# Kernel tuning notes

Measured on AMD Instinct MI355X. Metric: run time of the kernel, lower is better.

The kernel has to match this reference:

```python
import jax, jax.numpy as jnp
import numpy as np

B = 16384
D_IN = 1024
D_OUT = 512
H1 = 4 * D_IN      # floor(layersDimentions[0]*inputDimention) = 4096
H3 = 4 * D_OUT     # floor(layersDimentions[1]*outputDimention) = 2048
H4 = 4 * D_OUT     # floor(layersDimentions[2]*outputDimention) = 2048
M = 256            # codebook size


def _linear_params(key, fan_in, fan_out):
    kw, kb = jax.random.split(key)
    bound = 1.0 / np.sqrt(fan_in)
    w = jax.random.uniform(kw, (fan_out, fan_in), jnp.float32, -bound, bound)
    b = jax.random.uniform(kb, (fan_out,), jnp.float32, -bound, bound)
    return w, b


def setup_inputs() -> dict:
    key = jax.random.key(0)
    ks = jax.random.split(key, 7)
    x = jax.random.normal(ks[0], (B, D_IN), jnp.float32)
    codebook = jnp.sort(jax.random.normal(ks[1], (M,), jnp.float32))
    w1, b1 = _linear_params(ks[2], D_IN, H1)
    w2, b2 = _linear_params(ks[3], H1, D_OUT)
    w3, b3 = _linear_params(ks[4], D_OUT, H3)
    w4, b4 = _linear_params(ks[5], H3, H4)
    w5, b5 = _linear_params(ks[6], H4, D_OUT)
    return {"x": x, "codebook": codebook,
            "w1": w1, "b1": b1, "w2": w2, "b2": b2,
            "w3": w3, "b3": b3, "w4": w4, "b4": b4,
            "w5": w5, "b5": b5}


def _quantize(x, codebook):
    # nearest codeword per scalar element: argmin_m |x - c_m|
    # x: [B, D], codebook: [M]
    d = jnp.abs(x[..., None] - codebook)          # [B, D, M]
    idx = jnp.argmin(d, axis=-1)                  # [B, D]
    return codebook[idx]


def reference(x, codebook, w1, b1, w2, b2, w3, b3, w4, b4, w5, b5):
    h = x @ w1.T + b1                # [B, H1]
    h = h @ w2.T + b2                # [B, D_OUT]
    h = _quantize(h, codebook)       # [B, D_OUT]
    h = h @ w3.T + b3                # [B, H3]
    h = h @ w4.T + b4                # [B, H4]
    return h @ w5.T + b5             # [B, D_OUT]
```

## Files before the change

kernel.cpp:

```cpp
#include <hip/hip_runtime.h>


typedef __bf16 v8bf __attribute__((ext_vector_type(8)));
typedef float  v4f  __attribute__((ext_vector_type(4)));

#define Bdim   16384
#define DIN    1024
#define DOUT   512
#define H1dim  4096
#define H3dim  2048
#define H4dim  2048

#define GLOBAL_AS __attribute__((address_space(1)))
#define LDS_AS    __attribute__((address_space(3)))

__device__ __forceinline__ void load16_to_lds(const __bf16* g, __bf16* l) {
  __builtin_amdgcn_global_load_lds((const GLOBAL_AS unsigned int*)g,
                                   (LDS_AS unsigned int*)l, 16, 0, 0);
}

__device__ __forceinline__ unsigned pack2bf(float a, float b) {
  return (unsigned)__builtin_bit_cast(unsigned short, (__bf16)a) |
         ((unsigned)__builtin_bit_cast(unsigned short, (__bf16)b) << 16);
}

__device__ __forceinline__ void transpose_body(const float* __restrict__ in,
                                               __bf16* __restrict__ out,
                                               int R, int C, int bx, int by,
                                               float (*tile)[33]) {
  const int c0 = bx * 32, r0 = by * 32;
  const int t = threadIdx.x, tr = t >> 5, tc = t & 31;
#pragma unroll
  for (int i = 0; i < 4; ++i)
    tile[tr + i * 8][tc] = in[(size_t)(r0 + tr + i * 8) * C + (c0 + tc)];
  __syncthreads();
#pragma unroll
  for (int i = 0; i < 4; ++i)
    out[(size_t)(c0 + tr + i * 8) * R + (r0 + tc)] = (__bf16)tile[tc][tr + i * 8];
}

__global__ void prep_kernel(const float* __restrict__ w1, __bf16* __restrict__ w1T,
                            const float* __restrict__ w4, __bf16* __restrict__ w4T,
                            const float* __restrict__ w3, __bf16* __restrict__ w3T,
                            const float* __restrict__ x, __bf16* __restrict__ xb) {
  __shared__ float tile[32][33];
  int b = blockIdx.x;
  if (b < 4096) {
    transpose_body(w1, w1T, H1dim, DIN, b & 31, b >> 5, tile);
  } else if (b < 8192) {
    b -= 4096;
    transpose_body(w4, w4T, H4dim, H3dim, b & 63, b >> 6, tile);
  } else if (b < 9216) {
    b -= 8192;
    transpose_body(w3, w3T, H3dim, DOUT, b & 15, b >> 4, tile);
  } else {
    const size_t i = (size_t)(b - 9216) * 2048 + (size_t)threadIdx.x * 8;
    float4 a = *(const float4*)&x[i];
    float4 c = *(const float4*)&x[i + 4];
    int4 o;
    o.x = pack2bf(a.x, a.y); o.y = pack2bf(a.z, a.w);
    o.z = pack2bf(c.x, c.y); o.w = pack2bf(c.z, c.w);
    *(int4*)&xb[i] = o;
  }
}

__device__ __forceinline__ void bias_body(int bb, const float* __restrict__ b1,
                                          const float* __restrict__ w2,
                                          const float* __restrict__ b2,
                                          const float* __restrict__ b3,
                                          const __bf16* __restrict__ WtT,
                                          const float* __restrict__ b4,
                                          const float* __restrict__ w5,
                                          const float* __restrict__ b5,
                                          float* __restrict__ ba, float* __restrict__ bc) {
  const int wave = threadIdx.x >> 6, lane = threadIdx.x & 63;
  if (bb < 128) {
    const int j = bb * 4 + wave;
    float s = 0.f;
    for (int k = lane; k < H1dim; k += 64) s += b1[k] * w2[(size_t)j * H1dim + k];
#pragma unroll
    for (int off = 32; off; off >>= 1) s += __shfl_xor(s, off, 64);
    if (lane == 0) ba[j] = s + b2[j];
  } else {
    const int j = (bb - 128) * 4 + wave;
    float s = 0.f;
    for (int k = lane; k < H4dim; k += 64)
      s += b3[k] * (float)WtT[(size_t)j * H4dim + k] + b4[k] * w5[(size_t)j * H4dim + k];
#pragma unroll
    for (int off = 32; off; off >>= 1) s += __shfl_xor(s, off, 64);
    if (lane == 0) bc[j] = s + b5[j];
  }
}

template <bool ABF16>
__device__ __forceinline__ void splitk_body(__bf16* As, __bf16* Bs,
                                            int bx, int by, int bz,
                                            const void* __restrict__ Ain,
                                            const __bf16* __restrict__ Bt,
                                            float* __restrict__ Cpart,
                                            int M, int N, int K, int Kchunk) {
  const int t = threadIdx.x;
  const int m0 = bx * 64, n0 = by * 64;
  const int kbeg = bz * Kchunk;
  const int lane = t & 63, wave = t >> 6;
  const int quad = lane >> 4, l15 = lane & 15;
  const int wm = (wave & 1) * 32, wn = (wave >> 1) * 32;

  v4f acc[2][2];
#pragma unroll
  for (int i = 0; i < 2; ++i)
#pragma unroll
    for (int j = 0; j < 2; ++j) acc[i][j] = (v4f){0.f, 0.f, 0.f, 0.f};

  const int r = t >> 2, c = (t & 3) * 8;
  for (int k0 = kbeg; k0 < kbeg + Kchunk; k0 += 32) {
    if constexpr (ABF16) {
      const __bf16* A = (const __bf16*)Ain;
      *(int4*)&As[r * 40 + c] = *(const int4*)&A[(size_t)(m0 + r) * K + (k0 + c)];
    } else {
      const float* A = (const float*)Ain;
#pragma unroll
      for (int p = 0; p < 2; ++p) {
        const int idx = p * 256 + t;
        const int row = idx >> 3, col = (idx & 7) * 4;
        float4 v = *(const float4*)&A[(size_t)(m0 + row) * K + (k0 + col)];
        uint2 o;
        o.x = pack2bf(v.x, v.y);
        o.y = pack2bf(v.z, v.w);
        *(uint2*)&As[row * 40 + col] = o;
      }
    }
    *(int4*)&Bs[r * 40 + c] = *(const int4*)&Bt[(size_t)(n0 + r) * K + (k0 + c)];
    __syncthreads();
    v8bf af[2], bfr[2];
#pragma unroll
    for (int i = 0; i < 2; ++i) {
      af[i]  = *(const v8bf*)&As[(wm + i * 16 + l15) * 40 + quad * 8];
      bfr[i] = *(const v8bf*)&Bs[(wn + i * 16 + l15) * 40 + quad * 8];
    }
#pragma unroll
    for (int i = 0; i < 2; ++i)
#pragma unroll
      for (int j = 0; j < 2; ++j)
        acc[i][j] = __builtin_amdgcn_mfma_f32_16x16x32_bf16(af[i], bfr[j], acc[i][j], 0, 0, 0);
    __syncthreads();
  }

  float* dst = Cpart + (size_t)bz * M * N;
#pragma unroll
  for (int i = 0; i < 2; ++i)
#pragma unroll
    for (int j = 0; j < 2; ++j)
#pragma unroll
      for (int r2 = 0; r2 < 4; ++r2) {
        const int gm = m0 + wm + i * 16 + quad * 4 + r2;
        const int gn = n0 + wn + j * 16 + l15;
        dst[(size_t)gm * N + gn] = acc[i][j][r2];
      }
}

__global__ __launch_bounds__(256, 4)
void fold12_kernel(const float* __restrict__ w2, const __bf16* __restrict__ w1T,
                   float* __restrict__ part1,
                   const float* __restrict__ w5, const __bf16* __restrict__ w4T,
                   float* __restrict__ part2) {
  __shared__ __align__(16) __bf16 As[64 * 40];
  __shared__ __align__(16) __bf16 Bs[64 * 40];
  int b = blockIdx.x;
  if (b < 1024) {
    splitk_body<false>(As, Bs, b & 7, (b >> 3) & 15, b >> 7,
                       w2, w1T, part1, DOUT, DIN, H1dim, H1dim / 8);
  } else {
    b -= 1024;
    splitk_body<false>(As, Bs, b & 7, (b >> 3) & 31, b >> 8,
                       w5, w4T, part2, DOUT, H3dim, H4dim, H4dim / 4);
  }
}

__global__ __launch_bounds__(256, 4)
void fold3_bias_kernel(const __bf16* __restrict__ WtT, const __bf16* __restrict__ w3T,
                       float* __restrict__ part,
                       const float* __restrict__ b1, const float* __restrict__ w2,
                       const float* __restrict__ b2, const float* __restrict__ b3,
                       const float* __restrict__ b4, const float* __restrict__ w5,
                       const float* __restrict__ b5,
                       float* __restrict__ ba, float* __restrict__ bc) {
  __shared__ __align__(16) __bf16 As[64 * 40];
  __shared__ __align__(16) __bf16 Bs[64 * 40];
  int b = blockIdx.x;
  if (b < 512) {
    splitk_body<true>(As, Bs, b & 7, (b >> 3) & 7, b >> 6,
                      WtT, w3T, part, DOUT, DOUT, H3dim, H3dim / 8);
  } else {
    bias_body(b - 512, b1, w2, b2, b3, WtT, b4, w5, b5, ba, bc);
  }
}

__device__ __forceinline__ void reduce_body(const float* __restrict__ part,
                                            __bf16* __restrict__ out, int MN4, int S, int i) {
  if (i >= MN4) return;
  const float4* p = reinterpret_cast<const float4*>(part);
  float4 s = p[i];
  for (int k = 1; k < S; ++k) {
    float4 v = p[(size_t)k * MN4 + i];
    s.x += v.x; s.y += v.y; s.z += v.z; s.w += v.w;
  }
  uint2 o;
  o.x = pack2bf(s.x, s.y);
  o.y = pack2bf(s.z, s.w);
  reinterpret_cast<uint2*>(out)[i] = o;
}

__global__ void reduce12_kernel(const float* __restrict__ part1, __bf16* __restrict__ WaT,
                                const float* __restrict__ part2, __bf16* __restrict__ WtT) {
  const int b = blockIdx.x, t = threadIdx.x;
  if (b < 512) reduce_body(part1, WaT, DOUT * DIN / 4, 8, b * 256 + t);
  else         reduce_body(part2, WtT, DOUT * H3dim / 4, 4, (b - 512) * 256 + t);
}

__global__ void reduce_cast_kernel(const float* __restrict__ part,
                                   __bf16* __restrict__ out, int MN4, int S) {
  int i = blockIdx.x * blockDim.x + threadIdx.x;
  reduce_body(part, out, MN4, S, i);
}

enum { MODE_Q = 1, MODE_OUT = 2 };

template <int MODE>
__global__ __launch_bounds__(256, 4)
void gemm_main_kernel(const __bf16* __restrict__ A, const __bf16* __restrict__ Bt,
                      void* __restrict__ Cout, const float* __restrict__ bias,
                      const float* __restrict__ codebook, int M, int N, int K) {
  __shared__ __align__(16) __bf16 As[128 * 64];
  __shared__ __align__(16) __bf16 Bs[64 * 64];
  __shared__ float cbs[256];

  const int t = threadIdx.x;
  const int m0 = blockIdx.x * 128;
  const int n0 = blockIdx.y * 64;
  if constexpr (MODE == MODE_Q) cbs[t] = codebook[t];

  const int lane = t & 63, wave = t >> 6;
  const int quad = lane >> 4, l15 = lane & 15;
  const int wm = (wave & 1) * 64, wn = (wave >> 1) * 32;

  const int lrow = lane >> 3;
  const int gcol = (((lane & 7) ^ lrow) * 8);

  const __bf16* gA = A  + (size_t)(m0 + 32 * wave + lrow) * K + gcol;
  const __bf16* gB = Bt + (size_t)(n0 + 16 * wave + lrow) * K + gcol;
  __bf16* lA = &As[32 * wave * 64];
  __bf16* lB = &Bs[16 * wave * 64];

  v4f acc[4][2];
#pragma unroll
  for (int i = 0; i < 4; ++i)
#pragma unroll
    for (int j = 0; j < 2; ++j) acc[i][j] = (v4f){0.f, 0.f, 0.f, 0.f};

  const int swz = l15 & 7;

  for (int k0 = 0; k0 < K; k0 += 64) {
#pragma unroll
    for (int p = 0; p < 4; ++p)
      load16_to_lds(gA + (size_t)(8 * p) * K + k0, lA + p * 512);
#pragma unroll
    for (int p = 0; p < 2; ++p)
      load16_to_lds(gB + (size_t)(8 * p) * K + k0, lB + p * 512);
    __syncthreads();

#pragma unroll
    for (int kk = 0; kk < 2; ++kk) {
      const int cch = ((kk * 4 + quad) ^ swz) * 8;
      v8bf af[4], bv[2];
#pragma unroll
      for (int i = 0; i < 4; ++i)
        af[i] = *(const v8bf*)&As[(wm + i * 16 + l15) * 64 + cch];
#pragma unroll
      for (int j = 0; j < 2; ++j)
        bv[j] = *(const v8bf*)&Bs[(wn + j * 16 + l15) * 64 + cch];
#pragma unroll
      for (int i = 0; i < 4; ++i)
#pragma unroll
        for (int j = 0; j < 2; ++j)
          acc[i][j] = __builtin_amdgcn_mfma_f32_16x16x32_bf16(af[i], bv[j], acc[i][j], 0, 0, 0);
    }
    __syncthreads();
  }

#pragma unroll
  for (int j = 0; j < 2; ++j) {
    const int gn = n0 + wn + j * 16 + l15;
    const float bj = bias[gn];
#pragma unroll
    for (int i = 0; i < 4; ++i) {
#pragma unroll
      for (int r = 0; r < 4; ++r) {
        const int gm = m0 + wm + i * 16 + quad * 4 + r;
        float v = acc[i][j][r] + bj;
        if constexpr (MODE == MODE_Q) {
          int idx = 0;
#pragma unroll
          for (int s = 128; s > 0; s >>= 1) {
            const int u = idx + s;
            if (cbs[u] <= v) idx = u;
          }
          float best = cbs[idx];
          if (idx < 255) {
            const float c1 = cbs[idx + 1];
            if (!(v - best <= c1 - v)) best = c1;
          }
          ((__bf16*)Cout)[(size_t)gm * N + gn] = (__bf16)best;
        } else {
          ((float*)Cout)[(size_t)gm * N + gn] = v;
        }
      }
    }
  }
}

extern "C" void kernel_launch(void* const* d_in, const int* in_sizes, int n_in,
                              void* d_out, int out_size, void* d_ws, size_t ws_size,
                              hipStream_t stream) {
  const float* x  = (const float*)d_in[0];
  const float* cb = (const float*)d_in[1];
  const float* w1 = (const float*)d_in[2];
  const float* b1 = (const float*)d_in[3];
  const float* w2 = (const float*)d_in[4];
  const float* b2 = (const float*)d_in[5];
  const float* w3 = (const float*)d_in[6];
  const float* b3 = (const float*)d_in[7];
  const float* w4 = (const float*)d_in[8];
  const float* b4 = (const float*)d_in[9];
  const float* w5 = (const float*)d_in[10];
  const float* b5 = (const float*)d_in[11];
  float* out = (float*)d_out;

  char* ws = (char*)d_ws;
  size_t off = 0;
  auto alloc = [&](size_t bytes) -> void* {
    void* p = ws + off;
    off = (off + bytes + 255) & ~(size_t)255;
    return p;
  };
  __bf16* w1T  = (__bf16*)alloc((size_t)DIN * H1dim * 2);
  __bf16* w4T  = (__bf16*)alloc((size_t)H3dim * H4dim * 2);
  __bf16* w3T  = (__bf16*)alloc((size_t)DOUT * H3dim * 2);
  __bf16* WaT  = (__bf16*)alloc((size_t)DOUT * DIN * 2);
  __bf16* WtT  = (__bf16*)alloc((size_t)DOUT * H3dim * 2);
  __bf16* WcT  = (__bf16*)alloc((size_t)DOUT * DOUT * 2);
  __bf16* q    = (__bf16*)alloc((size_t)Bdim * DOUT * 2);
  float*  ba   = (float*)alloc(DOUT * 4);
  float*  bc   = (float*)alloc(DOUT * 4);
  float*  part1 = (float*)alloc((size_t)8 * DOUT * DIN * 4);
  __bf16* xb   = (__bf16*)alloc((size_t)Bdim * DIN * 2);
  float*  part2 = (float*)q;

  prep_kernel<<<9216 + 8192, 256, 0, stream>>>(w1, w1T, w4, w4T, w3, w3T, x, xb);

  fold12_kernel<<<2048, 256, 0, stream>>>(w2, w1T, part1, w5, w4T, part2);

  reduce12_kernel<<<1536, 256, 0, stream>>>(part1, WaT, part2, WtT);

  fold3_bias_kernel<<<768, 256, 0, stream>>>(WtT, w3T, part1,
                                             b1, w2, b2, b3, b4, w5, b5, ba, bc);

  reduce_cast_kernel<<<256, 256, 0, stream>>>(part1, WcT, DOUT * DOUT / 4, 8);

  gemm_main_kernel<MODE_Q><<<dim3(Bdim / 128, DOUT / 64), 256, 0, stream>>>(
      xb, WaT, q, ba, cb, Bdim, DOUT, DIN);

  gemm_main_kernel<MODE_OUT><<<dim3(Bdim / 128, DOUT / 64), 256, 0, stream>>>(
      q, WcT, out, bc, nullptr, Bdim, DOUT, DOUT);
}
```

Before: 304.1 us.

## Replace split-K weight folding with double-buffered full-K GEMMs and merge launches

Cuts the pipeline from seven launches to four. The split-K partial buffers and separate reduce kernels are replaced by a full-K MFMA GEMM that keeps chunked accumulators in registers and writes bf16 directly. w2 and w5 are pre-cast to bf16 in the prep kernel, and the transpose now uses 64-row tiles with vectorized stores. The main GEMMs gain a two-stage LDS double buffer, and the quantize GEMM shares a launch with the WcT fold and the bc bias computation. The trade-off is fewer blocks on the fold GEMMs, so less parallelism, plus more LDS per block.

New measurement: 291.0 us. 1.05x faster.

```diff
diff --git a/kernel.cpp b/kernel.cpp
--- a/kernel.cpp
+++ b/kernel.cpp
@@ -27,278 +27,189 @@
 __device__ __forceinline__ void transpose_body(const float* __restrict__ in,
                                                __bf16* __restrict__ out,
                                                int R, int C, int bx, int by,
-                                               float (*tile)[33]) {
-  const int c0 = bx * 32, r0 = by * 32;
+                                               float (*tile)[68]) {
+  const int c0 = bx * 32, r0 = by * 64;
   const int t = threadIdx.x, tr = t >> 5, tc = t & 31;
 #pragma unroll
-  for (int i = 0; i < 4; ++i)
-    tile[tr + i * 8][tc] = in[(size_t)(r0 + tr + i * 8) * C + (c0 + tc)];
+  for (int i = 0; i < 8; ++i)
+    tile[tc][tr + i * 8] = in[(size_t)(r0 + tr + i * 8) * C + (c0 + tc)];
   __syncthreads();
-#pragma unroll
-  for (int i = 0; i < 4; ++i)
-    out[(size_t)(c0 + tr + i * 8) * R + (r0 + tc)] = (__bf16)tile[tc][tr + i * 8];
+  const int orow = t >> 3, oc = (t & 7) * 8;
+  float4 a = *(const float4*)&tile[orow][oc];
+  float4 b = *(const float4*)&tile[orow][oc + 4];
+  int4 o;
+  o.x = pack2bf(a.x, a.y); o.y = pack2bf(a.z, a.w);
+  o.z = pack2bf(b.x, b.y); o.w = pack2bf(b.z, b.w);
+  *(int4*)&out[(size_t)(c0 + orow) * R + (r0 + oc)] = o;
+}
+
+__device__ __forceinline__ void cast_body(const float* __restrict__ in,
+                                          __bf16* __restrict__ out, int b) {
+  const size_t i = (size_t)b * 2048 + (size_t)threadIdx.x * 8;
+  float4 a = *(const float4*)&in[i];
+  float4 c = *(const float4*)&in[i + 4];
+  int4 o;
+  o.x = pack2bf(a.x, a.y); o.y = pack2bf(a.z, a.w);
+  o.z = pack2bf(c.x, c.y); o.w = pack2bf(c.z, c.w);
+  *(int4*)&out[i] = o;
 }
 
 __global__ void prep_kernel(const float* __restrict__ w1, __bf16* __restrict__ w1T,
                             const float* __restrict__ w4, __bf16* __restrict__ w4T,
                             const float* __restrict__ w3, __bf16* __restrict__ w3T,
-                            const float* __restrict__ x, __bf16* __restrict__ xb) {
-  __shared__ float tile[32][33];
+                            const float* __restrict__ x, __bf16* __restrict__ xb,
+                            const float* __restrict__ w2, __bf16* __restrict__ w2b,
+                            const float* __restrict__ w5, __bf16* __restrict__ w5b) {
+  __shared__ float tile[32][68];
   int b = blockIdx.x;
-  if (b < 4096) {
+  if (b < 2048) {
     transpose_body(w1, w1T, H1dim, DIN, b & 31, b >> 5, tile);
-  } else if (b < 8192) {
+  } else if (b < 4096) {
+    b -= 2048;
+    transpose_body(w4, w4T, H4dim, H3dim, b & 63, b >> 6, tile);
+  } else if (b < 4608) {
     b -= 4096;
-    transpose_body(w4, w4T, H4dim, H3dim, b & 63, b >> 6, tile);
-  } else if (b < 9216) {
-    b -= 8192;
     transpose_body(w3, w3T, H3dim, DOUT, b & 15, b >> 4, tile);
+  } else if (b < 12800) {
+    cast_body(x, xb, b - 4608);
+  } else if (b < 13824) {
+    cast_body(w2, w2b, b - 12800);
   } else {
-    const size_t i = (size_t)(b - 9216) * 2048 + (size_t)threadIdx.x * 8;
-    float4 a = *(const float4*)&x[i];
-    float4 c = *(const float4*)&x[i + 4];
-    int4 o;
-    o.x = pack2bf(a.x, a.y); o.y = pack2bf(a.z, a.w);
-    o.z = pack2bf(c.x, c.y); o.w = pack2bf(c.z, c.w);
-    *(int4*)&xb[i] = o;
-  }
-}
-
-__device__ __forceinline__ void bias_body(int bb, const float* __restrict__ b1,
-                                          const float* __restrict__ w2,
-                                          const float* __restrict__ b2,
-                                          const float* __restrict__ b3,
-                                          const __bf16* __restrict__ WtT,
-                                          const float* __restrict__ b4,
-                                          const float* __restrict__ w5,
-                                          const float* __restrict__ b5,
-                                          float* __restrict__ ba, float* __restrict__ bc) {
+    cast_body(w5, w5b, b - 13824);
+  }
+}
+
+__device__ __forceinline__ void bias_ba_body(int bb, const float* __restrict__ b1,
+                                             const float* __restrict__ w2,
+                                             const float* __restrict__ b2,
+                                             float* __restrict__ ba) {
   const int wave = threadIdx.x >> 6, lane = threadIdx.x & 63;
-  if (bb < 128) {
-    const int j = bb * 4 + wave;
-    float s = 0.f;
-    for (int k = lane; k < H1dim; k += 64) s += b1[k] * w2[(size_t)j * H1dim + k];
-#pragma unroll
-    for (int off = 32; off; off >>= 1) s += __shfl_xor(s, off, 64);
-    if (lane == 0) ba[j] = s + b2[j];
-  } else {
-    const int j = (bb - 128) * 4 + wave;
-    float s = 0.f;
-    for (int k = lane; k < H4dim; k += 64)
-      s += b3[k] * (float)WtT[(size_t)j * H4dim + k] + b4[k] * w5[(size_t)j * H4dim + k];
-#pragma unroll
-    for (int off = 32; off; off >>= 1) s += __shfl_xor(s, off, 64);
-    if (lane == 0) bc[j] = s + b5[j];
-  }
-}
-
-template <bool ABF16>
-__device__ __forceinline__ void splitk_body(__bf16* As, __bf16* Bs,
-                                            int bx, int by, int bz,
-                                            const void* __restrict__ Ain,
-                                            const __bf16* __restrict__ Bt,
-                                            float* __restrict__ Cpart,
-                                            int M, int N, int K, int Kchunk) {
+  const int j = bb * 4 + wave;
+  float s = 0.f;
+  for (int k = lane; k < H1dim; k += 64) s += b1[k] * w2[(size_t)j * H1dim + k];
+#pragma unroll
+  for (int off = 32; off; off >>= 1) s += __shfl_xor(s, off, 64);
+  if (lane == 0) ba[j] = s + b2[j];
+}
+
+__device__ __forceinline__ void bias_bc_body(int bb, const float* __restrict__ b3,
+                                             const __bf16* __restrict__ WtT,
+                                             const float* __restrict__ b4,
+                                             const float* __restrict__ w5,
+                                             const float* __restrict__ b5,
+                                             float* __restrict__ bc) {
+  const int wave = threadIdx.x >> 6, lane = threadIdx.x & 63;
+  const int j = bb * 4 + wave;
+  float s = 0.f;
+  for (int k = lane; k < H4dim; k += 64)
+    s += b3[k] * (float)WtT[(size_t)j * H4dim + k] + b4[k] * w5[(size_t)j * H4dim + k];
+#pragma unroll
+  for (int off = 32; off; off >>= 1) s += __shfl_xor(s, off, 64);
+  if (lane == 0) bc[j] = s + b5[j];
+}
+
+enum { MODE_W = 0, MODE_Q = 1, MODE_OUT = 2 };
+
+template <int MODE, int BM>
+__device__ __forceinline__ void gemm_body(__bf16* As, __bf16* Bs, float* cbs,
+                                          int bx, int by,
+                                          const __bf16* __restrict__ A,
+                                          const __bf16* __restrict__ Bt,
+                                          void* __restrict__ Cout,
+                                          const float* __restrict__ bias,
+                                          const float* __restrict__ codebook,
+                                          int M, int N, int K, int CH) {
   const int t = threadIdx.x;
-  const int m0 = bx * 64, n0 = by * 64;
-  const int kbeg = bz * Kchunk;
+  const int m0 = bx * BM, n0 = by * 64;
+  if constexpr (MODE == MODE_Q) cbs[t] = codebook[t];
+
   const int lane = t & 63, wave = t >> 6;
   const int quad = lane >> 4, l15 = lane & 15;
-  const int wm = (wave & 1) * 32, wn = (wave >> 1) * 32;
-
-  v4f acc[2][2];
-#pragma unroll
-  for (int i = 0; i < 2; ++i)
-#pragma unroll
-    for (int j = 0; j < 2; ++j) acc[i][j] = (v4f){0.f, 0.f, 0.f, 0.f};
-
-  const int r = t >> 2, c = (t & 3) * 8;
-  for (int k0 = kbeg; k0 < kbeg + Kchunk; k0 += 32) {
-    if constexpr (ABF16) {
-      const __bf16* A = (const __bf16*)Ain;
-      *(int4*)&As[r * 40 + c] = *(const int4*)&A[(size_t)(m0 + r) * K + (k0 + c)];
-    } else {
-      const float* A = (const float*)Ain;
-#pragma unroll
-      for (int p = 0; p < 2; ++p) {
-        const int idx = p * 256 + t;
-        const int row = idx >> 3, col = (idx & 7) * 4;
-        float4 v = *(const float4*)&A[(size_t)(m0 + row) * K + (k0 + col)];
-        uint2 o;
-        o.x = pack2bf(v.x, v.y);
-        o.y = pack2bf(v.z, v.w);
-        *(uint2*)&As[row * 40 + col] = o;
-      }
+  constexpr int MI = BM / 32;
+  const int wm = (wave & 1) * (BM / 2), wn = (wave >> 1) * 32;
+
+  const int lrow = lane >> 3;
+  const int gcol = ((lane & 7) ^ lrow) * 8;
+  const __bf16* gA = A  + (size_t)(m0 + (BM / 4) * wave + lrow) * K + gcol;
+  const __bf16* gB = Bt + (size_t)(n0 + 16 * wave + lrow) * K + gcol;
+  const int swz = l15 & 7;
+
+  v4f acc[MI][2], accT[MI][2];
+#pragma unroll
+  for (int i = 0; i < MI; ++i)
+#pragma unroll
+    for (int j = 0; j < 2; ++j) {
+      acc[i][j] = (v4f){0.f, 0.f, 0.f, 0.f};
+      if constexpr (MODE == MODE_W) accT[i][j] = (v4f){0.f, 0.f, 0.f, 0.f};
     }
-    *(int4*)&Bs[r * 40 + c] = *(const int4*)&Bt[(size_t)(n0 + r) * K + (k0 + c)];
-    __syncthreads();
-    v8bf af[2], bfr[2];
-#pragma unroll
-    for (int i = 0; i < 2; ++i) {
-      af[i]  = *(const v8bf*)&As[(wm + i * 16 + l15) * 40 + quad * 8];
-      bfr[i] = *(const v8bf*)&Bs[(wn + i * 16 + l15) * 40 + quad * 8];
-    }
-#pragma unroll
-    for (int i = 0; i < 2; ++i)
-#pragma unroll
-      for (int j = 0; j < 2; ++j)
-        acc[i][j] = __builtin_amdgcn_mfma_f32_16x16x32_bf16(af[i], bfr[j], acc[i][j], 0, 0, 0);
-    __syncthreads();
-  }
-
-  float* dst = Cpart + (size_t)bz * M * N;
-#pragma unroll
-  for (int i = 0; i < 2; ++i)
-#pragma unroll
-    for (int j = 0; j < 2; ++j)
-#pragma unroll
-      for (int r2 = 0; r2 < 4; ++r2) {
-        const int gm = m0 + wm + i * 16 + quad * 4 + r2;
-        const int gn = n0 + wn + j * 16 + l15;
-        dst[(size_t)gm * N + gn] = acc[i][j][r2];
-      }
-}
-
-__global__ __launch_bounds__(256, 4)
-void fold12_kernel(const float* __restrict__ w2, const __bf16* __restrict__ w1T,
-                   float* __restrict__ part1,
-                   const float* __restrict__ w5, const __bf16* __restrict__ w4T,
-                   float* __restrict__ part2) {
-  __shared__ __align__(16) __bf16 As[64 * 40];
-  __shared__ __align__(16) __bf16 Bs[64 * 40];
-  int b = blockIdx.x;
-  if (b < 1024) {
-    splitk_body<false>(As, Bs, b & 7, (b >> 3) & 15, b >> 7,
-                       w2, w1T, part1, DOUT, DIN, H1dim, H1dim / 8);
-  } else {
-    b -= 1024;
-    splitk_body<false>(As, Bs, b & 7, (b >> 3) & 31, b >> 8,
-                       w5, w4T, part2, DOUT, H3dim, H4dim, H4dim / 4);
-  }
-}
-
-__global__ __launch_bounds__(256, 4)
-void fold3_bias_kernel(const __bf16* __restrict__ WtT, const __bf16* __restrict__ w3T,
-                       float* __restrict__ part,
-                       const float* __restrict__ b1, const float* __restrict__ w2,
-                       const float* __restrict__ b2, const float* __restrict__ b3,
-                       const float* __restrict__ b4, const float* __restrict__ w5,
-                       const float* __restrict__ b5,
-                       float* __restrict__ ba, float* __restrict__ bc) {
-  __shared__ __align__(16) __bf16 As[64 * 40];
-  __shared__ __align__(16) __bf16 Bs[64 * 40];
-  int b = blockIdx.x;
-  if (b < 512) {
-    splitk_body<true>(As, Bs, b & 7, (b >> 3) & 7, b >> 6,
-                      WtT, w3T, part, DOUT, DOUT, H3dim, H3dim / 8);
-  } else {
-    bias_body(b - 512, b1, w2, b2, b3, WtT, b4, w5, b5, ba, bc);
-  }
-}
-
-__device__ __forceinline__ void reduce_body(const float* __restrict__ part,
-                                            __bf16* __restrict__ out, int MN4, int S, int i) {
-  if (i >= MN4) return;
-  const float4* p = reinterpret_cast<const float4*>(part);
-  float4 s = p[i];
-  for (int k = 1; k < S; ++k) {
-    float4 v = p[(size_t)k * MN4 + i];
-    s.x += v.x; s.y += v.y; s.z += v.z; s.w += v.w;
-  }
-  uint2 o;
-  o.x = pack2bf(s.x, s.y);
-  o.y = pack2bf(s.z, s.w);
-  reinterpret_cast<uint2*>(out)[i] = o;
-}
-
-__global__ void reduce12_kernel(const float* __restrict__ part1, __bf16* __restrict__ WaT,
-                                const float* __restrict__ part2, __bf16* __restrict__ WtT) {
-  const int b = blockIdx.x, t = threadIdx.x;
-  if (b < 512) reduce_body(part1, WaT, DOUT * DIN / 4, 8, b * 256 + t);
-  else         reduce_body(part2, WtT, DOUT * H3dim / 4, 4, (b - 512) * 256 + t);
-}
-
-__global__ void reduce_cast_kernel(const float* __restrict__ part,
-                                   __bf16* __restrict__ out, int MN4, int S) {
-  int i = blockIdx.x * blockDim.x + threadIdx.x;
-  reduce_body(part, out, MN4, S, i);
-}
-
-enum { MODE_Q = 1, MODE_OUT = 2 };
-
-template <int MODE>
-__global__ __launch_bounds__(256, 4)
-void gemm_main_kernel(const __bf16* __restrict__ A, const __bf16* __restrict__ Bt,
-                      void* __restrict__ Cout, const float* __restrict__ bias,
-                      const float* __restrict__ codebook, int M, int N, int K) {
-  __shared__ __align__(16) __bf16 As[128 * 64];
-  __shared__ __align__(16) __bf16 Bs[64 * 64];
-  __shared__ float cbs[256];
-
-  const int t = threadIdx.x;
-  const int m0 = blockIdx.x * 128;
-  const int n0 = blockIdx.y * 64;
-  if constexpr (MODE == MODE_Q) cbs[t] = codebook[t];
-
-  const int lane = t & 63, wave = t >> 6;
-  const int quad = lane >> 4, l15 = lane & 15;
-  const int wm = (wave & 1) * 64, wn = (wave >> 1) * 32;
-
-  const int lrow = lane >> 3;
-  const int gcol = (((lane & 7) ^ lrow) * 8);
-
-  const __bf16* gA = A  + (size_t)(m0 + 32 * wave + lrow) * K + gcol;
-  const __bf16* gB = Bt + (size_t)(n0 + 16 * wave + lrow) * K + gcol;
-  __bf16* lA = &As[32 * wave * 64];
-  __bf16* lB = &Bs[16 * wave * 64];
-
-  v4f acc[4][2];
-#pragma unroll
-  for (int i = 0; i < 4; ++i)
-#pragma unroll
-    for (int j = 0; j < 2; ++j) acc[i][j] = (v4f){0.f, 0.f, 0.f, 0.f};
-
-  const int swz = l15 & 7;
-
-  for (int k0 = 0; k0 < K; k0 += 64) {
-#pragma unroll
-    for (int p = 0; p < 4; ++p)
+
+  auto stage = [&](int k0, int buf) {
+    __bf16* lA = As + buf * (BM * 64) + (BM / 4) * wave * 64;
+    __bf16* lB = Bs + buf * (64 * 64) + 16 * wave * 64;
+#pragma unroll
+    for (int p = 0; p < MI; ++p)
       load16_to_lds(gA + (size_t)(8 * p) * K + k0, lA + p * 512);
 #pragma unroll
     for (int p = 0; p < 2; ++p)
       load16_to_lds(gB + (size_t)(8 * p) * K + k0, lB + p * 512);
-    __syncthreads();
-
+  };
+
+  stage(0, 0);
+  __syncthreads();
+
+  const int nk = K >> 6;
+  const int chsteps = CH >> 6;
+  int cc = 0, buf = 0;
+  for (int tk = 0; tk < nk; ++tk) {
+    if (tk + 1 < nk) stage((tk + 1) << 6, buf ^ 1);
+    const __bf16* cA = As + buf * (BM * 64);
+    const __bf16* cB = Bs + buf * (64 * 64);
 #pragma unroll
     for (int kk = 0; kk < 2; ++kk) {
       const int cch = ((kk * 4 + quad) ^ swz) * 8;
-      v8bf af[4], bv[2];
-#pragma unroll
-      for (int i = 0; i < 4; ++i)
-        af[i] = *(const v8bf*)&As[(wm + i * 16 + l15) * 64 + cch];
+      v8bf af[MI], bv[2];
+#pragma unroll
+      for (int i = 0; i < MI; ++i)
+        af[i] = *(const v8bf*)&cA[(wm + i * 16 + l15) * 64 + cch];
 #pragma unroll
       for (int j = 0; j < 2; ++j)
-        bv[j] = *(const v8bf*)&Bs[(wn + j * 16 + l15) * 64 + cch];
-#pragma unroll
-      for (int i = 0; i < 4; ++i)
+        bv[j] = *(const v8bf*)&cB[(wn + j * 16 + l15) * 64 + cch];
+#pragma unroll
+      for (int i = 0; i < MI; ++i)
 #pragma unroll
         for (int j = 0; j < 2; ++j)
           acc[i][j] = __builtin_amdgcn_mfma_f32_16x16x32_bf16(af[i], bv[j], acc[i][j], 0, 0, 0);
     }
+    if constexpr (MODE == MODE_W) {
+      if (++cc == chsteps) {
+        cc = 0;
+#pragma unroll
+        for (int i = 0; i < MI; ++i)
+#pragma unroll
+          for (int j = 0; j < 2; ++j) {
+            accT[i][j] += acc[i][j];
+            acc[i][j] = (v4f){0.f, 0.f, 0.f, 0.f};
+          }
+      }
+    }
     __syncthreads();
+    buf ^= 1;
   }
 
 #pragma unroll
   for (int j = 0; j < 2; ++j) {
     const int gn = n0 + wn + j * 16 + l15;
-    const float bj = bias[gn];
-#pragma unroll
-    for (int i = 0; i < 4; ++i) {
+    float bj = 0.f;
+    if constexpr (MODE != MODE_W) bj = bias[gn];
+#pragma unroll
+    for (int i = 0; i < MI; ++i) {
 #pragma unroll
       for (int r = 0; r < 4; ++r) {
         const int gm = m0 + wm + i * 16 + quad * 4 + r;
-        float v = acc[i][j][r] + bj;
-        if constexpr (MODE == MODE_Q) {
+        if constexpr (MODE == MODE_W) {
+          ((__bf16*)Cout)[(size_t)gm * N + gn] = (__bf16)accT[i][j][r];
+        } else if constexpr (MODE == MODE_Q) {
+          float v = acc[i][j][r] + bj;
           int idx = 0;
 #pragma unroll
           for (int s = 128; s > 0; s >>= 1) {
@@ -312,11 +223,67 @@
           }
           ((__bf16*)Cout)[(size_t)gm * N + gn] = (__bf16)best;
         } else {
-          ((float*)Cout)[(size_t)gm * N + gn] = v;
+          ((float*)Cout)[(size_t)gm * N + gn] = acc[i][j][r] + bj;
         }
       }
     }
   }
+}
+
+__global__ __launch_bounds__(256, 3)
+void foldA_kernel(const __bf16* __restrict__ w2b, const __bf16* __restrict__ w1T,
+                  __bf16* __restrict__ WaT,
+                  const __bf16* __restrict__ w5b, const __bf16* __restrict__ w4T,
+                  __bf16* __restrict__ WtT,
+                  const float* __restrict__ b1, const float* __restrict__ w2,
+                  const float* __restrict__ b2, float* __restrict__ ba) {
+  __shared__ __align__(16) __bf16 As[2 * 64 * 64];
+  __shared__ __align__(16) __bf16 Bs[2 * 64 * 64];
+  int b = blockIdx.x;
+  if (b < 128) {
+    gemm_body<MODE_W, 64>(As, Bs, nullptr, b & 7, b >> 3, w2b, w1T, WaT,
+                          nullptr, nullptr, DOUT, DIN, H1dim, 512);
+  } else if (b < 384) {
+    b -= 128;
+    gemm_body<MODE_W, 64>(As, Bs, nullptr, b & 7, b >> 3, w5b, w4T, WtT,
+                          nullptr, nullptr, DOUT, H3dim, H4dim, 512);
+  } else {
+    bias_ba_body(b - 384, b1, w2, b2, ba);
+  }
+}
+
+__global__ __launch_bounds__(256, 3)
+void foldB_kernel(const __bf16* __restrict__ WtT, const __bf16* __restrict__ w3T,
+                  __bf16* __restrict__ WcT,
+                  const float* __restrict__ b3, const float* __restrict__ b4,
+                  const float* __restrict__ w5, const float* __restrict__ b5,
+                  float* __restrict__ bc,
+                  const __bf16* __restrict__ xb, const __bf16* __restrict__ WaT,
+                  __bf16* __restrict__ q, const float* __restrict__ ba,
+                  const float* __restrict__ cb) {
+  __shared__ __align__(16) __bf16 As[2 * 128 * 64];
+  __shared__ __align__(16) __bf16 Bs[2 * 64 * 64];
+  __shared__ float cbs[256];
+  int b = blockIdx.x;
+  if (b < 64) {
+    gemm_body<MODE_W, 64>(As, Bs, nullptr, b & 7, b >> 3, WtT, w3T, WcT,
+                          nullptr, nullptr, DOUT, DOUT, H3dim, 256);
+  } else if (b < 192) {
+    bias_bc_body(b - 64, b3, WtT, b4, w5, b5, bc);
+  } else {
+    b -= 192;
+    gemm_body<MODE_Q, 128>(As, Bs, cbs, b & 127, b >> 7, xb, WaT, q,
+                           ba, cb, Bdim, DOUT, DIN, DIN);
+  }
+}
+
+__global__ __launch_bounds__(256, 3)
+void gemmout_kernel(const __bf16* __restrict__ q, const __bf16* __restrict__ WcT,
+                    float* __restrict__ out, const float* __restrict__ bc) {
+  __shared__ __align__(16) __bf16 As[2 * 128 * 64];
+  __shared__ __align__(16) __bf16 Bs[2 * 64 * 64];
+  gemm_body<MODE_OUT, 128>(As, Bs, nullptr, blockIdx.x & 127, blockIdx.x >> 7,
+                           q, WcT, out, bc, nullptr, Bdim, DOUT, DOUT, DOUT);
 }
 
 extern "C" void kernel_launch(void* const* d_in, const int* in_sizes, int n_in,
@@ -343,33 +310,27 @@
     off = (off + bytes + 255) & ~(size_t)255;
     return p;
   };
-  __bf16* w1T  = (__bf16*)alloc((size_t)DIN * H1dim * 2);
-  __bf16* w4T  = (__bf16*)alloc((size_t)H3dim * H4dim * 2);
-  __bf16* w3T  = (__bf16*)alloc((size_t)DOUT * H3dim * 2);
-  __bf16* WaT  = (__bf16*)alloc((size_t)DOUT * DIN * 2);
-  __bf16* WtT  = (__bf16*)alloc((size_t)DOUT * H3dim * 2);
-  __bf16* WcT  = (__bf16*)alloc((size_t)DOUT * DOUT * 2);
-  __bf16* q    = (__bf16*)alloc((size_t)Bdim * DOUT * 2);
-  float*  ba   = (float*)alloc(DOUT * 4);
-  float*  bc   = (float*)alloc(DOUT * 4);
-  float*  part1 = (float*)alloc((size_t)8 * DOUT * DIN * 4);
-  __bf16* xb   = (__bf16*)alloc((size_t)Bdim * DIN * 2);
-  float*  part2 = (float*)q;
-
-  prep_kernel<<<9216 + 8192, 256, 0, stream>>>(w1, w1T, w4, w4T, w3, w3T, x, xb);
-
-  fold12_kernel<<<2048, 256, 0, stream>>>(w2, w1T, part1, w5, w4T, part2);
-
-  reduce12_kernel<<<1536, 256, 0, stream>>>(part1, WaT, part2, WtT);
-
-  fold3_bias_kernel<<<768, 256, 0, stream>>>(WtT, w3T, part1,
-                                             b1, w2, b2, b3, b4, w5, b5, ba, bc);
-
-  reduce_cast_kernel<<<256, 256, 0, stream>>>(part1, WcT, DOUT * DOUT / 4, 8);
-
-  gemm_main_kernel<MODE_Q><<<dim3(Bdim / 128, DOUT / 64), 256, 0, stream>>>(
-      xb, WaT, q, ba, cb, Bdim, DOUT, DIN);
-
-  gemm_main_kernel<MODE_OUT><<<dim3(Bdim / 128, DOUT / 64), 256, 0, stream>>>(
-      q, WcT, out, bc, nullptr, Bdim, DOUT, DOUT);
-}
+  __bf16* w1T = (__bf16*)alloc((size_t)DIN * H1dim * 2);
+  __bf16* w4T = (__bf16*)alloc((size_t)H3dim * H4dim * 2);
+  __bf16* w3T = (__bf16*)alloc((size_t)DOUT * H3dim * 2);
+  __bf16* w2b = (__bf16*)alloc((size_t)DOUT * H1dim * 2);
+  __bf16* w5b = (__bf16*)alloc((size_t)DOUT * H4dim * 2);
+  __bf16* WaT = (__bf16*)alloc((size_t)DOUT * DIN * 2);
+  __bf16* WtT = (__bf16*)alloc((size_t)DOUT * H3dim * 2);
+  __bf16* WcT = (__bf16*)alloc((size_t)DOUT * DOUT * 2);
+  __bf16* q   = (__bf16*)alloc((size_t)Bdim * DOUT * 2);
+  __bf16* xb  = (__bf16*)alloc((size_t)Bdim * DIN * 2);
+  float*  ba  = (float*)alloc(DOUT * 4);
+  float*  bc  = (float*)alloc(DOUT * 4);
+
+  prep_kernel<<<14336, 256, 0, stream>>>(w1, w1T, w4, w4T, w3, w3T,
+                                         x, xb, w2, w2b, w5, w5b);
+
+  foldA_kernel<<<512, 256, 0, stream>>>(w2b, w1T, WaT, w5b, w4T, WtT,
+                                        b1, w2, b2, ba);
+
+  foldB_kernel<<<1216, 256, 0, stream>>>(WtT, w3T, WcT, b3, b4, w5, b5, bc,
+                                         xb, WaT, q, ba, cb);
+
+  gemmout_kernel<<<1024, 256, 0, stream>>>(q, WcT, out, bc);
+}
```
